# Kernel optimization log

Measured on AMD Instinct MI355X. Metric: run time of the kernel, lower is better.

## Reference

```python
import jax, jax.numpy as jnp
import numpy as np

N_NODES = 100000
N_EDGES = 100000
NNZ = 1600000
C_IN = 128
C_OUT = 128


def setup_inputs() -> dict:
    key = jax.random.key(0)
    k1, k2, k3, k4, k5 = jax.random.split(key, 5)
    x_0 = jax.random.normal(k1, (N_NODES, C_IN), dtype=jnp.float32)
    node_idx = jax.random.randint(k2, (NNZ,), 0, N_NODES, dtype=jnp.int64)
    edge_idx = jnp.sort(jax.random.randint(k3, (NNZ,), 0, N_EDGES, dtype=jnp.int64))
    values = jnp.ones((NNZ,), dtype=jnp.float32)
    weight = jax.random.normal(k4, (C_IN, C_OUT), dtype=jnp.float32) * (1.0 / np.sqrt(C_IN))
    att_weight = jax.random.normal(k5, (2 * C_IN, 1), dtype=jnp.float32) * 0.1
    return {"x_0": x_0, "node_idx": node_idx, "edge_idx": edge_idx,
            "values": values, "weight": weight, "att_weight": att_weight}


def reference(x_0, node_idx, edge_idx, values, weight, att_weight):
    # Step 1: m_0_1 = B1^T @ x_0  -> hyperedge features [n_edges, C_in]
    m_0_1 = jax.ops.segment_sum(values[:, None] * x_0[node_idx], edge_idx,
                                num_segments=N_EDGES)
    # Attention per nonzero (node i, hyperedge j):
    # elu(cat(m_0_1[j], x_0[i]) @ att_weight)  == elu((m01@a_src)[j] + (x0@a_tgt)[i])
    a_src = att_weight[:C_IN, 0]
    a_tgt = att_weight[C_IN:, 0]
    scores = jax.nn.elu((m_0_1 @ a_src)[edge_idx] + (x_0 @ a_tgt)[node_idx])  # [nnz]
    # x_message = m_0_1 @ Theta
    x_message = m_0_1 @ weight  # [n_edges, C_out]
    # Attention-weighted scatter back to nodes: (B1 * att) @ x_message
    out = jax.ops.segment_sum((scores * values)[:, None] * x_message[edge_idx],
                              node_idx, num_segments=N_NODES)
    return out
```

## Files before the change

### kernel.cpp

```cpp
#include <hip/hip_runtime.h>
#include <math.h>

#define N_NODES 100000
#define N_EDGES 100000
#define NNZT    1600000
#define C       128
#define NB      ((N_NODES + 255) >> 8)
#define EPB     8192

typedef _Float16 half8 __attribute__((ext_vector_type(8)));
typedef _Float16 h2    __attribute__((ext_vector_type(2)));
typedef float    f32x4 __attribute__((ext_vector_type(4)));

__global__ __launch_bounds__(256) void k1_node_dot(
    const float* __restrict__ x0, const float* __restrict__ att,
    float* __restrict__ t_node, _Float16* __restrict__ x0h)
{
    int wave = threadIdx.x >> 6;
    int lane = threadIdx.x & 63;
    int node = blockIdx.x * 4 + wave;
    const float2 xv = *reinterpret_cast<const float2*>(x0 + (size_t)node * C + lane * 2);
    h2 hx = { (_Float16)xv.x, (_Float16)xv.y };
    *reinterpret_cast<h2*>(x0h + (size_t)node * C + lane * 2) = hx;
    const float2 av = *reinterpret_cast<const float2*>(att + C + lane * 2);
    float v = xv.x * av.x + xv.y * av.y;
    #pragma unroll
    for (int off = 32; off > 0; off >>= 1) v += __shfl_xor(v, off, 64);
    if (lane == 0) t_node[node] = v;
}

__global__ __launch_bounds__(256) void k_rowptr(
    const int* __restrict__ edge_idx, int* __restrict__ row_start)
{
    int e = blockIdx.x * 256 + threadIdx.x;
    if (e >= NNZT) return;
    int j = edge_idx[e];
    int jprev = (e == 0) ? -1 : edge_idx[e - 1];
    for (int k = jprev + 1; k <= j; ++k) row_start[k] = e;
    if (e == NNZT - 1)
        for (int k = j + 1; k <= N_EDGES; ++k) row_start[k] = NNZT;
}

__global__ __launch_bounds__(256) void k_wcvt(
    const float* __restrict__ W, _Float16* __restrict__ wt)
{
    int i = blockIdx.x * 256 + threadIdx.x;
    int k = i >> 7, n = i & 127;
    wt[(size_t)n * C + k] = (_Float16)W[(size_t)k * C + n];
}

__global__ __launch_bounds__(256) void k2_edge_msg(
    const half8* __restrict__ x0h,
    const int*   __restrict__ node_idx,
    const int*   __restrict__ row_start,
    const float* __restrict__ values,
    const float* __restrict__ att,
    _Float16* __restrict__ m01h,
    float* __restrict__ s_edge)
{
    int wave = threadIdx.x >> 6;
    int lane = threadIdx.x & 63;
    int j    = blockIdx.x * 4 + wave;
    int sub  = lane >> 4;
    int ln   = lane & 15;
    int start = row_start[j];
    int end   = row_start[j + 1];

    h2 hacc[4];
    #pragma unroll
    for (int q = 0; q < 4; ++q) hacc[q] = (h2){(_Float16)0.f, (_Float16)0.f};

    int e = start + sub;
    for (; e + 4 < end; e += 8) {
        int   n0 = node_idx[e];
        int   n1 = node_idx[e + 4];
        _Float16 v0 = (_Float16)values[e];
        _Float16 v1 = (_Float16)values[e + 4];
        h2 v0p = {v0, v0}, v1p = {v1, v1};
        half8 A = x0h[(size_t)n0 * 16 + ln];
        half8 B = x0h[(size_t)n1 * 16 + ln];
        const h2* a2 = reinterpret_cast<const h2*>(&A);
        const h2* b2 = reinterpret_cast<const h2*>(&B);
        #pragma unroll
        for (int q = 0; q < 4; ++q)
            hacc[q] = a2[q] * v0p + (b2[q] * v1p + hacc[q]);
    }
    if (e < end) {
        int   n0 = node_idx[e];
        _Float16 v0 = (_Float16)values[e];
        h2 v0p = {v0, v0};
        half8 A = x0h[(size_t)n0 * 16 + ln];
        const h2* a2 = reinterpret_cast<const h2*>(&A);
        #pragma unroll
        for (int q = 0; q < 4; ++q) hacc[q] = a2[q] * v0p + hacc[q];
    }

    float f[8];
    #pragma unroll
    for (int q = 0; q < 4; ++q) {
        f[2 * q]     = (float)hacc[q][0];
        f[2 * q + 1] = (float)hacc[q][1];
    }
    #pragma unroll
    for (int q = 0; q < 8; ++q) {
        f[q] += __shfl_xor(f[q], 16, 64);
        f[q] += __shfl_xor(f[q], 32, 64);
    }
    if (lane < 16) {
        half8 hv;
        #pragma unroll
        for (int q = 0; q < 8; ++q) hv[q] = (_Float16)f[q];
        reinterpret_cast<half8*>(m01h + (size_t)j * C)[ln] = hv;
    }
    f32x4 a0 = *reinterpret_cast<const f32x4*>(att + ln * 8);
    f32x4 a1 = *reinterpret_cast<const f32x4*>(att + ln * 8 + 4);
    float p = f[0] * a0[0] + f[1] * a0[1] + f[2] * a0[2] + f[3] * a0[3]
            + f[4] * a1[0] + f[5] * a1[1] + f[6] * a1[2] + f[7] * a1[3];
    #pragma unroll
    for (int off = 8; off > 0; off >>= 1) p += __shfl_xor(p, off, 64);
    if (lane == 0) s_edge[j] = p;
}

__global__ __launch_bounds__(256) void k_bhist(
    const int* __restrict__ node_idx, int* __restrict__ btot)
{
    __shared__ int cnt4[4][NB];
    int tid = threadIdx.x;
    int w   = tid >> 6;
    for (int b = tid; b < 4 * NB; b += 256) (&cnt4[0][0])[b] = 0;
    __syncthreads();
    const int per = (NNZT + 255) / 256;
    int e0 = blockIdx.x * per;
    int e1 = e0 + per; if (e1 > NNZT) e1 = NNZT;
    for (int e = e0 + tid; e < e1; e += 256)
        atomicAdd(&cnt4[w][node_idx[e] >> 8], 1);
    __syncthreads();
    for (int b = tid; b < NB; b += 256) {
        int cc = cnt4[0][b] + cnt4[1][b] + cnt4[2][b] + cnt4[3][b];
        if (cc) atomicAdd(&btot[b], cc);
    }
}

__global__ __launch_bounds__(512) void k_bscan(
    const int* __restrict__ btot, int* __restrict__ bbase, int* __restrict__ bcur)
{
    __shared__ int s[512];
    int tid = threadIdx.x;
    int v = (tid < NB) ? btot[tid] : 0;
    s[tid] = v;
    __syncthreads();
    for (int off = 1; off < 512; off <<= 1) {
        int t = (tid >= off) ? s[tid - off] : 0;
        __syncthreads();
        s[tid] += t;
        __syncthreads();
    }
    if (tid < NB) { bbase[tid] = s[tid] - v; bcur[tid] = s[tid] - v; }
    if (tid == NB - 1) bbase[NB] = s[tid];
}

__global__ __launch_bounds__(256) void k_binA(
    const int*   __restrict__ node_idx,
    const int*   __restrict__ edge_idx,
    const float* __restrict__ values,
    const float* __restrict__ s_edge,
    const float* __restrict__ t_node,
    int*  __restrict__ bcur,
    int*  __restrict__ tmp_n,
    int2* __restrict__ tmp_jc)
{
    __shared__ int cnt4[4][NB];
    __shared__ int res4[4][NB];
    int tid = threadIdx.x;
    int w   = tid >> 6;
    for (int b = tid; b < 4 * NB; b += 256) (&cnt4[0][0])[b] = 0;
    __syncthreads();
    int e0 = blockIdx.x * EPB;
    int e1 = e0 + EPB; if (e1 > NNZT) e1 = NNZT;
    for (int e = e0 + tid; e < e1; e += 256)
        atomicAdd(&cnt4[w][node_idx[e] >> 8], 1);
    __syncthreads();
    for (int b = tid; b < NB; b += 256) {
        int c0 = cnt4[0][b], c1 = cnt4[1][b], c2 = cnt4[2][b], c3 = cnt4[3][b];
        int tot = c0 + c1 + c2 + c3;
        int r = tot ? atomicAdd(&bcur[b], tot) : 0;
        res4[0][b] = r;
        res4[1][b] = r + c0;
        res4[2][b] = r + c0 + c1;
        res4[3][b] = r + c0 + c1 + c2;
        cnt4[0][b] = 0; cnt4[1][b] = 0; cnt4[2][b] = 0; cnt4[3][b] = 0;
    }
    __syncthreads();
    for (int e = e0 + tid; e < e1; e += 256) {
        int n = node_idx[e];
        int b = n >> 8;
        int r = atomicAdd(&cnt4[w][b], 1);
        int pos = res4[w][b] + r;
        int j = edge_idx[e];
        float s = s_edge[j] + t_node[n];
        float coef = (s > 0.f ? s : expm1f(s)) * values[e];
        tmp_n[pos]  = n;
        tmp_jc[pos] = make_int2(j, __float_as_int(coef));
    }
}

__global__ __launch_bounds__(256) void k_binB(
    const int*  __restrict__ tmp_n,
    const int2* __restrict__ tmp_jc,
    const int*  __restrict__ bbase,
    int*  __restrict__ base,
    int*  __restrict__ count,
    int2* __restrict__ jc)
{
    int b   = blockIdx.x;
    int tid = threadIdx.x;
    int n0  = b << 8;
    __shared__ int cnt[256], scn[256], cur[256];
    __shared__ int lo_s, hi_s;
    cnt[tid] = 0;
    if (tid == 0) { lo_s = bbase[b]; hi_s = bbase[b + 1]; }
    __syncthreads();
    int lo = lo_s, hi = hi_s;
    for (int i = lo + tid; i < hi; i += 256)
        atomicAdd(&cnt[tmp_n[i] - n0], 1);
    __syncthreads();
    int v = cnt[tid];
    scn[tid] = v;
    __syncthreads();
    for (int off = 1; off < 256; off <<= 1) {
        int t = (tid >= off) ? scn[tid - off] : 0;
        __syncthreads();
        scn[tid] += t;
        __syncthreads();
    }
    int excl = scn[tid] - v;
    int nn = n0 + tid;
    if (nn < N_NODES) { base[nn] = lo + excl; count[nn] = v; }
    cur[tid] = lo + excl;
    __syncthreads();
    for (int i = lo + tid; i < hi; i += 256) {
        int n = tmp_n[i];
        int pos = atomicAdd(&cur[n - n0], 1);
        jc[pos] = tmp_jc[i];
    }
}

__global__ __launch_bounds__(256) void k3_gather(
    const half8* __restrict__ m01h,
    const int2*  __restrict__ jc,
    const int*   __restrict__ base,
    const int*   __restrict__ count,
    _Float16* __restrict__ yh)
{
    int wave = threadIdx.x >> 6;
    int lane = threadIdx.x & 63;
    int n    = blockIdx.x * 4 + wave;
    int sub  = lane >> 4;
    int ln   = lane & 15;
    int b    = base[n];
    int cnt  = count[n];

    float facc[8];
    #pragma unroll
    for (int q = 0; q < 8; ++q) facc[q] = 0.f;

    int i = sub;
    for (; i + 4 < cnt; i += 8) {
        int2 p0 = jc[b + i];
        int2 p1 = jc[b + i + 4];
        float c0 = __int_as_float(p0.y);
        float c1 = __int_as_float(p1.y);
        half8 a  = m01h[(size_t)p0.x * 16 + ln];
        half8 bb = m01h[(size_t)p1.x * 16 + ln];
        #pragma unroll
        for (int q = 0; q < 8; ++q)
            facc[q] += c0 * (float)a[q] + c1 * (float)bb[q];
    }
    if (i < cnt) {
        int2 p0 = jc[b + i];
        float c0 = __int_as_float(p0.y);
        half8 a = m01h[(size_t)p0.x * 16 + ln];
        #pragma unroll
        for (int q = 0; q < 8; ++q) facc[q] += c0 * (float)a[q];
    }

    #pragma unroll
    for (int q = 0; q < 8; ++q) {
        facc[q] += __shfl_xor(facc[q], 16, 64);
        facc[q] += __shfl_xor(facc[q], 32, 64);
    }
    if (lane < 16) {
        half8 hv;
        #pragma unroll
        for (int q = 0; q < 8; ++q) hv[q] = (_Float16)facc[q];
        reinterpret_cast<half8*>(yh + (size_t)n * C)[ln] = hv;
    }
}

__global__ __launch_bounds__(64) void k4_mfma(
    const _Float16* __restrict__ yh,
    const _Float16* __restrict__ wt,
    float* __restrict__ out)
{
    int lane = threadIdx.x;
    int m    = lane & 15;
    int quad = lane >> 4;
    int rb   = blockIdx.x * 16;
    const _Float16* yrow = yh + (size_t)(rb + m) * C + quad * 8;
    half8 a[4];
    #pragma unroll
    for (int kc = 0; kc < 4; ++kc)
        a[kc] = *reinterpret_cast<const half8*>(yrow + kc * 32);
    #pragma unroll
    for (int ct = 0; ct < 8; ++ct) {
        const _Float16* wrow = wt + (size_t)(ct * 16 + m) * C + quad * 8;
        f32x4 acc = {0.f, 0.f, 0.f, 0.f};
        #pragma unroll
        for (int kc = 0; kc < 4; ++kc) {
            half8 b = *reinterpret_cast<const half8*>(wrow + kc * 32);
            acc = __builtin_amdgcn_mfma_f32_16x16x32_f16(a[kc], b, acc, 0, 0, 0);
        }
        int orow = rb + quad * 4;
        int ocol = ct * 16 + m;
        #pragma unroll
        for (int r = 0; r < 4; ++r)
            out[(size_t)(orow + r) * C + ocol] = acc[r];
    }
}

extern "C" void kernel_launch(void* const* d_in, const int* in_sizes, int n_in,
                              void* d_out, int out_size, void* d_ws, size_t ws_size,
                              hipStream_t stream)
{
    const float* x0       = (const float*)d_in[0];
    const int*   node_idx = (const int*)  d_in[1];
    const int*   edge_idx = (const int*)  d_in[2];
    const float* values   = (const float*)d_in[3];
    const float* W        = (const float*)d_in[4];
    const float* att      = (const float*)d_in[5];
    float* out = (float*)d_out;

    _Float16* x0h_s  = (_Float16*)d_out;
    _Float16* m01h_s = x0h_s + (size_t)N_NODES * C;
    int*  tmp_n  = (int*)d_out;
    int2* tmp_jc = (int2*)((char*)d_out + (size_t)NNZT * 4);

    char*  p   = (char*)d_ws;
    _Float16* yh    = (_Float16*)p; p += (size_t)N_NODES * C * sizeof(_Float16);
    float* t_node   = (float*)p;  p += N_NODES * sizeof(float);
    float* s_edge   = (float*)p;  p += N_EDGES * sizeof(float);
    int*   count    = (int*)p;    p += N_NODES * sizeof(int);
    int*   base     = (int*)p;    p += N_NODES * sizeof(int);
    int*   btot     = (int*)p;    p += 512 * sizeof(int);
    int*   bbase    = (int*)p;    p += 512 * sizeof(int);
    int*   bcur     = (int*)p;    p += 512 * sizeof(int);
    int*   row_start= (int*)p;    p += (N_EDGES + 1) * sizeof(int);
    _Float16* wt    = (_Float16*)p; p += (size_t)C * C * sizeof(_Float16);
    int2*  jc       = (int2*)p;   p += (size_t)NNZT * sizeof(int2);

    hipMemsetAsync(btot, 0, NB * sizeof(int), stream);

    k1_node_dot<<<N_NODES / 4, 256, 0, stream>>>(x0, att, t_node, x0h_s);
    k_rowptr<<<(NNZT + 255) / 256, 256, 0, stream>>>(edge_idx, row_start);
    k_wcvt  <<<(C * C + 255) / 256, 256, 0, stream>>>(W, wt);
    k2_edge_msg<<<N_EDGES / 4, 256, 0, stream>>>((const half8*)x0h_s, node_idx, row_start,
                                                 values, att, m01h_s, s_edge);

    k_bhist<<<256, 256, 0, stream>>>(node_idx, btot);
    k_bscan<<<1, 512, 0, stream>>>(btot, bbase, bcur);
    k_binA<<<(NNZT + EPB - 1) / EPB, 256, 0, stream>>>(node_idx, edge_idx, values,
                                                       s_edge, t_node, bcur, tmp_n, tmp_jc);
    k_binB<<<NB, 256, 0, stream>>>(tmp_n, tmp_jc, bbase, base, count, jc);

    k3_gather<<<N_NODES / 4, 256, 0, stream>>>((const half8*)m01h_s, jc, base, count, yh);
    k4_mfma<<<N_NODES / 16, 64, 0, stream>>>(yh, wt, out);
}
```

Baseline: 370.1 us.

## Fuse node binning and gather into bucket-level partition and gather kernels

```diff
diff --git a/kernel.cpp b/kernel.cpp
--- a/kernel.cpp
+++ b/kernel.cpp
@@ -6,7 +6,8 @@
 #define NNZT    1600000
 #define C       128
 #define NB      ((N_NODES + 255) >> 8)
-#define EPB     8192
+#define CHUNK   4096
+#define ORDCAP  6144
 
 typedef _Float16 half8 __attribute__((ext_vector_type(8)));
 typedef _Float16 h2    __attribute__((ext_vector_type(2)));
@@ -159,141 +160,150 @@
     if (tid == NB - 1) bbase[NB] = s[tid];
 }
 
-__global__ __launch_bounds__(256) void k_binA(
+__global__ __launch_bounds__(512) void k_part(
     const int*   __restrict__ node_idx,
     const int*   __restrict__ edge_idx,
     const float* __restrict__ values,
     const float* __restrict__ s_edge,
     const float* __restrict__ t_node,
     int*  __restrict__ bcur,
-    int*  __restrict__ tmp_n,
-    int2* __restrict__ tmp_jc)
-{
-    __shared__ int cnt4[4][NB];
-    __shared__ int res4[4][NB];
+    int2* __restrict__ rec)
+{
+    __shared__ int hist[NB];
+    __shared__ int lbase[NB];
+    __shared__ int gb[NB];
+    __shared__ int cur[NB];
+    __shared__ int2 lrec[CHUNK];
+    __shared__ unsigned short lbid[CHUNK];
     int tid = threadIdx.x;
-    int w   = tid >> 6;
-    for (int b = tid; b < 4 * NB; b += 256) (&cnt4[0][0])[b] = 0;
-    __syncthreads();
-    int e0 = blockIdx.x * EPB;
-    int e1 = e0 + EPB; if (e1 > NNZT) e1 = NNZT;
-    for (int e = e0 + tid; e < e1; e += 256)
-        atomicAdd(&cnt4[w][node_idx[e] >> 8], 1);
-    __syncthreads();
-    for (int b = tid; b < NB; b += 256) {
-        int c0 = cnt4[0][b], c1 = cnt4[1][b], c2 = cnt4[2][b], c3 = cnt4[3][b];
-        int tot = c0 + c1 + c2 + c3;
-        int r = tot ? atomicAdd(&bcur[b], tot) : 0;
-        res4[0][b] = r;
-        res4[1][b] = r + c0;
-        res4[2][b] = r + c0 + c1;
-        res4[3][b] = r + c0 + c1 + c2;
-        cnt4[0][b] = 0; cnt4[1][b] = 0; cnt4[2][b] = 0; cnt4[3][b] = 0;
-    }
-    __syncthreads();
-    for (int e = e0 + tid; e < e1; e += 256) {
+    int e0 = blockIdx.x * CHUNK;
+    int m = NNZT - e0; if (m > CHUNK) m = CHUNK;
+
+    for (int b = tid; b < NB; b += 512) hist[b] = 0;
+    __syncthreads();
+    for (int i = tid; i < m; i += 512)
+        atomicAdd(&hist[node_idx[e0 + i] >> 8], 1);
+    __syncthreads();
+    int c = (tid < NB) ? hist[tid] : 0;
+    for (int off = 1; off < NB; off <<= 1) {
+        int t = 0;
+        if (tid < NB && tid >= off) t = hist[tid - off];
+        __syncthreads();
+        if (tid < NB) hist[tid] += t;
+        __syncthreads();
+    }
+    if (tid < NB) {
+        int excl = hist[tid] - c;
+        lbase[tid] = excl;
+        cur[tid]   = excl;
+        gb[tid]    = c ? atomicAdd(&bcur[tid], c) : 0;
+    }
+    __syncthreads();
+    for (int i = tid; i < m; i += 512) {
+        int e = e0 + i;
         int n = node_idx[e];
         int b = n >> 8;
-        int r = atomicAdd(&cnt4[w][b], 1);
-        int pos = res4[w][b] + r;
         int j = edge_idx[e];
+        float v = values[e];
         float s = s_edge[j] + t_node[n];
-        float coef = (s > 0.f ? s : expm1f(s)) * values[e];
-        tmp_n[pos]  = n;
-        tmp_jc[pos] = make_int2(j, __float_as_int(coef));
-    }
-}
-
-__global__ __launch_bounds__(256) void k_binB(
-    const int*  __restrict__ tmp_n,
-    const int2* __restrict__ tmp_jc,
-    const int*  __restrict__ bbase,
-    int*  __restrict__ base,
-    int*  __restrict__ count,
-    int2* __restrict__ jc)
-{
-    int b   = blockIdx.x;
-    int tid = threadIdx.x;
-    int n0  = b << 8;
-    __shared__ int cnt[256], scn[256], cur[256];
-    __shared__ int lo_s, hi_s;
-    cnt[tid] = 0;
-    if (tid == 0) { lo_s = bbase[b]; hi_s = bbase[b + 1]; }
-    __syncthreads();
-    int lo = lo_s, hi = hi_s;
-    for (int i = lo + tid; i < hi; i += 256)
-        atomicAdd(&cnt[tmp_n[i] - n0], 1);
-    __syncthreads();
-    int v = cnt[tid];
-    scn[tid] = v;
+        float coef = (s > 0.f ? s : expm1f(s)) * v;
+        int slot = atomicAdd(&cur[b], 1);
+        lrec[slot] = make_int2(((n & 255) << 17) | j, __float_as_int(coef));
+        lbid[slot] = (unsigned short)b;
+    }
+    __syncthreads();
+    for (int s = tid; s < m; s += 512) {
+        int b = lbid[s];
+        rec[gb[b] + (s - lbase[b])] = lrec[s];
+    }
+}
+
+__global__ __launch_bounds__(512) void k_bgather(
+    const int2*  __restrict__ rec,
+    const int*   __restrict__ bbase,
+    const half8* __restrict__ m01h,
+    _Float16* __restrict__ yh)
+{
+    __shared__ int cnt[256];
+    __shared__ int bl[256];
+    __shared__ int cur[256];
+    __shared__ unsigned short ord[ORDCAP];
+    int b = blockIdx.x, tid = threadIdx.x;
+    int lo = bbase[b], hi = bbase[b + 1];
+    int m = hi - lo;
+    int mm = m < ORDCAP ? m : ORDCAP;
+
+    if (tid < 256) cnt[tid] = 0;
+    __syncthreads();
+    for (int i = tid; i < mm; i += 512)
+        atomicAdd(&cnt[((unsigned)rec[lo + i].x) >> 17], 1);
+    __syncthreads();
+    if (tid < 256) bl[tid] = cnt[tid];
     __syncthreads();
     for (int off = 1; off < 256; off <<= 1) {
-        int t = (tid >= off) ? scn[tid - off] : 0;
-        __syncthreads();
-        scn[tid] += t;
-        __syncthreads();
-    }
-    int excl = scn[tid] - v;
-    int nn = n0 + tid;
-    if (nn < N_NODES) { base[nn] = lo + excl; count[nn] = v; }
-    cur[tid] = lo + excl;
-    __syncthreads();
-    for (int i = lo + tid; i < hi; i += 256) {
-        int n = tmp_n[i];
-        int pos = atomicAdd(&cur[n - n0], 1);
-        jc[pos] = tmp_jc[i];
-    }
-}
-
-__global__ __launch_bounds__(256) void k3_gather(
-    const half8* __restrict__ m01h,
-    const int2*  __restrict__ jc,
-    const int*   __restrict__ base,
-    const int*   __restrict__ count,
-    _Float16* __restrict__ yh)
-{
-    int wave = threadIdx.x >> 6;
-    int lane = threadIdx.x & 63;
-    int n    = blockIdx.x * 4 + wave;
-    int sub  = lane >> 4;
-    int ln   = lane & 15;
-    int b    = base[n];
-    int cnt  = count[n];
-
-    float facc[8];
-    #pragma unroll
-    for (int q = 0; q < 8; ++q) facc[q] = 0.f;
-
-    int i = sub;
-    for (; i + 4 < cnt; i += 8) {
-        int2 p0 = jc[b + i];
-        int2 p1 = jc[b + i + 4];
-        float c0 = __int_as_float(p0.y);
-        float c1 = __int_as_float(p1.y);
-        half8 a  = m01h[(size_t)p0.x * 16 + ln];
-        half8 bb = m01h[(size_t)p1.x * 16 + ln];
-        #pragma unroll
-        for (int q = 0; q < 8; ++q)
-            facc[q] += c0 * (float)a[q] + c1 * (float)bb[q];
-    }
-    if (i < cnt) {
-        int2 p0 = jc[b + i];
-        float c0 = __int_as_float(p0.y);
-        half8 a = m01h[(size_t)p0.x * 16 + ln];
-        #pragma unroll
-        for (int q = 0; q < 8; ++q) facc[q] += c0 * (float)a[q];
-    }
-
-    #pragma unroll
-    for (int q = 0; q < 8; ++q) {
-        facc[q] += __shfl_xor(facc[q], 16, 64);
-        facc[q] += __shfl_xor(facc[q], 32, 64);
-    }
-    if (lane < 16) {
-        half8 hv;
-        #pragma unroll
-        for (int q = 0; q < 8; ++q) hv[q] = (_Float16)facc[q];
-        reinterpret_cast<half8*>(yh + (size_t)n * C)[ln] = hv;
+        int t = 0;
+        if (tid < 256 && tid >= off) t = bl[tid - off];
+        __syncthreads();
+        if (tid < 256) bl[tid] += t;
+        __syncthreads();
+    }
+    if (tid < 256) cur[tid] = bl[tid] - cnt[tid];
+    __syncthreads();
+    for (int i = tid; i < mm; i += 512) {
+        int local = ((unsigned)rec[lo + i].x) >> 17;
+        int p = atomicAdd(&cur[local], 1);
+        ord[p] = (unsigned short)i;
+    }
+    __syncthreads();
+
+    int wave = tid >> 6, lane = tid & 63, sub = lane >> 4, ln = lane & 15;
+    for (int local = wave; local < 256; local += 8) {
+        int n = (b << 8) + local;
+        if (n >= N_NODES) break;
+        int cb = bl[local] - cnt[local];
+        int cc = cnt[local];
+        float facc[8];
+        #pragma unroll
+        for (int q = 0; q < 8; ++q) facc[q] = 0.f;
+        int i = sub;
+        for (; i + 4 < cc; i += 8) {
+            int2 r0 = rec[lo + ord[cb + i]];
+            int2 r1 = rec[lo + ord[cb + i + 4]];
+            half8 a0 = m01h[(size_t)(r0.x & 0x1FFFF) * 16 + ln];
+            half8 a1 = m01h[(size_t)(r1.x & 0x1FFFF) * 16 + ln];
+            float c0 = __int_as_float(r0.y);
+            float c1 = __int_as_float(r1.y);
+            #pragma unroll
+            for (int q = 0; q < 8; ++q)
+                facc[q] += c0 * (float)a0[q] + c1 * (float)a1[q];
+        }
+        if (i < cc) {
+            int2 r0 = rec[lo + ord[cb + i]];
+            half8 a0 = m01h[(size_t)(r0.x & 0x1FFFF) * 16 + ln];
+            float c0 = __int_as_float(r0.y);
+            #pragma unroll
+            for (int q = 0; q < 8; ++q) facc[q] += c0 * (float)a0[q];
+        }
+        for (int x = ORDCAP + sub; x < m; x += 4) {
+            int2 r = rec[lo + x];
+            if ((int)(((unsigned)r.x) >> 17) == local) {
+                float c0 = __int_as_float(r.y);
+                half8 a0 = m01h[(size_t)(r.x & 0x1FFFF) * 16 + ln];
+                #pragma unroll
+                for (int q = 0; q < 8; ++q) facc[q] += c0 * (float)a0[q];
+            }
+        }
+        #pragma unroll
+        for (int q = 0; q < 8; ++q) {
+            facc[q] += __shfl_xor(facc[q], 16, 64);
+            facc[q] += __shfl_xor(facc[q], 32, 64);
+        }
+        if (lane < 16) {
+            half8 hv;
+            #pragma unroll
+            for (int q = 0; q < 8; ++q) hv[q] = (_Float16)facc[q];
+            reinterpret_cast<half8*>(yh + (size_t)n * C)[ln] = hv;
+        }
     }
 }
 
@@ -342,21 +352,17 @@
 
     _Float16* x0h_s  = (_Float16*)d_out;
     _Float16* m01h_s = x0h_s + (size_t)N_NODES * C;
-    int*  tmp_n  = (int*)d_out;
-    int2* tmp_jc = (int2*)((char*)d_out + (size_t)NNZT * 4);
+    int2* rec = (int2*)d_out;
 
     char*  p   = (char*)d_ws;
     _Float16* yh    = (_Float16*)p; p += (size_t)N_NODES * C * sizeof(_Float16);
     float* t_node   = (float*)p;  p += N_NODES * sizeof(float);
     float* s_edge   = (float*)p;  p += N_EDGES * sizeof(float);
-    int*   count    = (int*)p;    p += N_NODES * sizeof(int);
-    int*   base     = (int*)p;    p += N_NODES * sizeof(int);
     int*   btot     = (int*)p;    p += 512 * sizeof(int);
     int*   bbase    = (int*)p;    p += 512 * sizeof(int);
     int*   bcur     = (int*)p;    p += 512 * sizeof(int);
     int*   row_start= (int*)p;    p += (N_EDGES + 1) * sizeof(int);
     _Float16* wt    = (_Float16*)p; p += (size_t)C * C * sizeof(_Float16);
-    int2*  jc       = (int2*)p;   p += (size_t)NNZT * sizeof(int2);
 
     hipMemsetAsync(btot, 0, NB * sizeof(int), stream);
 
@@ -368,10 +374,8 @@
 
     k_bhist<<<256, 256, 0, stream>>>(node_idx, btot);
     k_bscan<<<1, 512, 0, stream>>>(btot, bbase, bcur);
-    k_binA<<<(NNZT + EPB - 1) / EPB, 256, 0, stream>>>(node_idx, edge_idx, values,
-                                                       s_edge, t_node, bcur, tmp_n, tmp_jc);
-    k_binB<<<NB, 256, 0, stream>>>(tmp_n, tmp_jc, bbase, base, count, jc);
-
-    k3_gather<<<N_NODES / 4, 256, 0, stream>>>((const half8*)m01h_s, jc, base, count, yh);
+    k_part <<<(NNZT + CHUNK - 1) / CHUNK, 512, 0, stream>>>(node_idx, edge_idx, values,
+                                                            s_edge, t_node, bcur, rec);
+    k_bgather<<<NB, 512, 0, stream>>>(rec, bbase, (const half8*)m01h_s, yh);
     k4_mfma<<<N_NODES / 16, 64, 0, stream>>>(yh, wt, out);
 }
```

New measurement: 358.3 us. 3.2% less time.
